# Kernel tuning notes

Measured on AMD Instinct MI355X. Metric: run time of the kernel, lower is better.

The kernel has to match this reference:

```python
import jax, jax.numpy as jnp
import numpy as np

N_HEAD, D_K, D_V, D_MODEL = 8, 64, 64, 512
LN_EPS = 1e-5

def setup_inputs() -> dict:
    key = jax.random.key(0)
    k1, k2, k3 = jax.random.split(key, 3)
    B, C, H, W = 8, D_MODEL, 32, 32
    q = jax.random.normal(k1, (B, C, H, W), dtype=jnp.float32)
    w_qkvs = jax.random.normal(k2, (N_HEAD * D_K, D_MODEL), dtype=jnp.float32) * np.sqrt(2.0 / (D_MODEL + D_K))
    fc_w = jax.random.normal(k3, (D_MODEL, N_HEAD * D_V), dtype=jnp.float32) * np.sqrt(2.0 / (N_HEAD * D_V + D_MODEL))
    fc_b = jnp.zeros((D_MODEL,), dtype=jnp.float32)
    ln_gamma = jnp.ones((D_MODEL,), dtype=jnp.float32)
    ln_beta = jnp.zeros((D_MODEL,), dtype=jnp.float32)
    return {"q": q, "w_qkvs": w_qkvs, "fc_w": fc_w, "fc_b": fc_b,
            "ln_gamma": ln_gamma, "ln_beta": ln_beta}

def reference(q, w_qkvs, fc_w, fc_b, ln_gamma, ln_beta):
    B, C, H, W = q.shape
    L = H * W
    temp = np.sqrt(D_K).astype(np.float32)
    # [B, C, H, W] -> [B, L, C] tokens
    x = q.reshape(B, C, L).transpose(0, 2, 1)
    residual = x
    # shared QKV projection -> per-head [B, h, L, d]
    qh = (x @ w_qkvs.T).reshape(B, L, N_HEAD, D_K).transpose(0, 2, 1, 3)
    # self-attention: q = k = v = qh
    scores = jnp.einsum('bhqd,bhkd->bhqk', qh, qh) / temp
    attn = jax.nn.softmax(scores, axis=-1)  # dropout is identity in eval
    out = jnp.einsum('bhqk,bhkd->bhqd', attn, qh)  # [B, h, L, d_v]
    # merge heads: [B, L, h*d_v]
    out = out.transpose(0, 2, 1, 3).reshape(B, L, N_HEAD * D_V)
    out = out @ fc_w.T + fc_b
    y = out + residual
    mu = jnp.mean(y, axis=-1, keepdims=True)
    var = jnp.mean(jnp.square(y - mu), axis=-1, keepdims=True)
    y = (y - mu) / jnp.sqrt(var + LN_EPS) * ln_gamma + ln_beta
    # raw reshape, matching torch .view(B, -1, H, W)
    return y.reshape(B, -1, H, W)
```

## Files before the change

kernel.cpp:

```cpp
#include <hip/hip_runtime.h>
#include <stdint.h>

#define BATCH 8
#define LTOK 1024
#define DMODEL 512
#define NHEAD 8
#define DHEAD 64

typedef unsigned short u16;
typedef u16 u16x4 __attribute__((ext_vector_type(4)));
typedef u16 u16x8 __attribute__((ext_vector_type(8)));
typedef short bf16x8 __attribute__((ext_vector_type(8)));
typedef float f32x4 __attribute__((ext_vector_type(4)));

#define MFMA16(a,b,c) __builtin_amdgcn_mfma_f32_16x16x32_bf16((a),(b),(c),0,0,0)

__device__ __forceinline__ float bf2f(u16 x){
  union{unsigned u; float f;} v; v.u = ((unsigned)x)<<16; return v.f;
}
__device__ __forceinline__ u16 f2bf(float f){
  union{float f; unsigned u;} v; v.f = f;
  unsigned r = v.u + 0x7fffu + ((v.u>>16)&1u);
  return (u16)(r>>16);
}

__device__ __forceinline__ void gload_lds16(const u16* g, u16* l){
  __builtin_amdgcn_global_load_lds(
      (const __attribute__((address_space(1))) void*)g,
      (__attribute__((address_space(3))) void*)l,
      16, 0, 0);
}

__global__ __launch_bounds__(256) void convert2_k(const float* __restrict__ s0,
                                                  u16* __restrict__ d0,
                                                  const float* __restrict__ s1,
                                                  u16* __restrict__ d1){
  const int blk = blockIdx.x;
  const float* src = (blk < 128) ? s0 : s1;
  u16* dst        = (blk < 128) ? d0 : d1;
  const int i = (((blk & 127)*256) + threadIdx.x)*8;
  u16x8 v;
  #pragma unroll
  for (int j=0;j<8;j++) v[j] = f2bf(src[i+j]);
  *(u16x8*)(dst + i) = v;
}

__global__ __launch_bounds__(256) void transpose_f2b(const float* __restrict__ src,
                                                     u16* __restrict__ dst,
                                                     int R, int C){
  __shared__ __align__(16) u16 t[64][72];
  const int b  = blockIdx.z;
  const int r0 = blockIdx.x*64, c0 = blockIdx.y*64;
  const float* s = src + (size_t)b*R*C;
  u16* d         = dst + (size_t)b*R*C;
  const int tid = threadIdx.x;
  const int row = tid>>3, ch = (tid&7)*8;
  #pragma unroll
  for (int rr=0; rr<64; rr+=32){
    const float* p = s + (size_t)(r0+row+rr)*C + c0 + ch;
    u16x8 v;
    #pragma unroll
    for (int j=0;j<8;j++) v[j] = f2bf(p[j]);
    *(u16x8*)&t[row+rr][ch] = v;
  }
  __syncthreads();
  #pragma unroll
  for (int rr=0; rr<64; rr+=32){
    const int dr = row+rr;
    u16x8 v;
    #pragma unroll
    for (int j=0;j<8;j++) v[j] = t[ch+j][dr];
    *(u16x8*)(d + (size_t)(c0+dr)*R + r0 + ch) = v;
  }
}

__device__ __forceinline__ void stage_gemm(const u16* __restrict__ src,
                                           int row0, int k0, u16* lds, int tid){
  #pragma unroll
  for (int s2=0; s2<2; ++s2){
    const int slot = tid + s2*256;
    const int row = slot>>3, ch8 = slot&7;
    const int k = k0 + ((ch8 ^ (row&7))<<3);
    gload_lds16(src + (size_t)(row0+row)*DMODEL + k, lds + slot*8);
  }
}

__global__ __launch_bounds__(256) void qkv_gemm(const u16* __restrict__ A,
                                                const u16* __restrict__ W,
                                                u16* __restrict__ Kf,
                                                u16* __restrict__ Vf){
  __shared__ __align__(128) u16 sA[2][4096];
  __shared__ __align__(128) u16 sB[2][4096];
  const int m0 = blockIdx.x*64, n0 = blockIdx.y*64;
  const int tid = threadIdx.x, w = tid>>6, lane = tid&63;
  const int wr = w>>1, wc = w&1;
  const int lr = lane&15, lg = lane>>4;
  f32x4 acc[2][2] = {};
  stage_gemm(A, m0, 0, sA[0], tid);
  stage_gemm(W, n0, 0, sB[0], tid);
  int buf = 0;
  for (int kt=0; kt<8; ++kt){
    __syncthreads();
    if (kt < 7){
      stage_gemm(A, m0, (kt+1)*64, sA[buf^1], tid);
      stage_gemm(W, n0, (kt+1)*64, sB[buf^1], tid);
    }
    #pragma unroll
    for (int ks=0; ks<2; ++ks){
      bf16x8 af[2], bfr[2];
      #pragma unroll
      for (int mi=0; mi<2; ++mi){
        const int r = wr*32 + mi*16 + lr;
        af[mi] = *(const bf16x8*)(&sA[buf][(r*64 + ks*32 + lg*8) ^ ((r&7)<<3)]);
      }
      #pragma unroll
      for (int nj=0; nj<2; ++nj){
        const int r = wc*32 + nj*16 + lr;
        bfr[nj] = *(const bf16x8*)(&sB[buf][(r*64 + ks*32 + lg*8) ^ ((r&7)<<3)]);
      }
      #pragma unroll
      for (int mi=0; mi<2; ++mi)
        #pragma unroll
        for (int nj=0; nj<2; ++nj)
          acc[mi][nj] = MFMA16(af[mi], bfr[nj], acc[mi][nj]);
    }
    buf ^= 1;
  }
  u16* lK = sA[0];
  u16* lV = sB[0];
  #pragma unroll
  for (int mi=0; mi<2; ++mi)
    #pragma unroll
    for (int nj=0; nj<2; ++nj){
      const int d   = wc*32 + nj*16 + lr;
      const int rr0 = wr*32 + mi*16 + lg*4;
      #pragma unroll
      for (int r=0; r<4; ++r){
        const int rr = rr0 + r;
        lK[((d>>5)*4 + (rr>>4))*512 + (((d>>3)&3)*16 + (rr&15))*8 + (d&7)]
            = f2bf(acc[mi][nj][r]);
      }
      u16x4 pv;
      #pragma unroll
      for (int r=0; r<4; ++r) pv[r] = f2bf(acc[mi][nj][r]);
      *(u16x4*)&lV[((rr0>>5)*4 + (d>>4))*512 + (((rr0>>3)&3)*16 + (d&15))*8 + (rr0&7)] = pv;
    }
  __syncthreads();
  const int bb = m0>>10, t = (m0&1023)>>6, hh = n0>>6;
  u16* Kt = Kf + (size_t)(((bb*NHEAD+hh)*16) + t)*4096;
  u16* Vt = Vf + (size_t)(((bb*NHEAD+hh)*16) + t)*4096;
  #pragma unroll
  for (int it=0; it<2; ++it){
    const int off = tid*8 + it*2048;
    *(u16x8*)(Kt + off) = *(const u16x8*)(lK + off);
    *(u16x8*)(Vt + off) = *(const u16x8*)(lV + off);
  }
}

__global__ __launch_bounds__(256,2) void attn_k(const u16* __restrict__ kf,
                                                const u16* __restrict__ vf,
                                                u16* __restrict__ ao){
  __shared__ __align__(16) u16 sPm[16640];
  const int bid = blockIdx.x;
  const int qt = bid >> 6, bh = bid & 63;
  const int b = bh >> 3, h = bh & 7;
  const u16* Kf = kf + (size_t)bh*16*4096;
  const u16* Vf = vf + (size_t)bh*16*4096;
  const int tid = threadIdx.x, w = tid>>6, lane = tid&63;
  const int lr = lane&15, lg = lane>>4;

  bf16x8 aq[4][2];
  #pragma unroll
  for (int g=0; g<4; ++g)
    #pragma unroll
    for (int ks=0; ks<2; ++ks){
      u16x8 v = *(const u16x8*)(Kf + (size_t)qt*4096 + (ks*4+g)*512 + lane*8);
      bf16x8 t;
      #pragma unroll
      for (int j=0;j<8;j++) t[j] = (short)f2bf(bf2f(v[j])*0.18033688f);
      aq[g][ks] = t;
    }

  f32x4 o[4][4] = {};
  float lsum[4][4] = {};

  for (int t=0; t<4; ++t){
    const int kt = w + t*4;
    const u16* Kt = Kf + (size_t)kt*4096;
    const u16* Vt = Vf + (size_t)kt*4096;
    bf16x8 bk[2][4];
    #pragma unroll
    for (int ks=0; ks<2; ++ks)
      #pragma unroll
      for (int nj=0; nj<4; ++nj)
        bk[ks][nj] = *(const bf16x8*)(Kt + (ks*4+nj)*512 + lane*8);
    #pragma unroll
    for (int g=0; g<4; ++g){
      f32x4 sc[4] = {};
      __builtin_amdgcn_s_setprio(1);
      #pragma unroll
      for (int ks=0; ks<2; ++ks)
        #pragma unroll
        for (int nj=0; nj<4; ++nj)
          sc[nj] = MFMA16(aq[g][ks], bk[ks][nj], sc[nj]);
      __builtin_amdgcn_s_setprio(0);
      const int wp = (w*4+g)*1024;
      #pragma unroll
      for (int nj=0; nj<4; ++nj){
        #pragma unroll
        for (int r=0; r<4; ++r){
          const float p = __builtin_amdgcn_exp2f(sc[nj][r]);
          const unsigned pu = __float_as_uint(p) & 0xFFFF0000u;
          lsum[g][r] += __uint_as_float(pu);
          const int prow = lg*4 + r;
          sPm[wp + ((prow*64 + nj*16 + lr) ^ ((prow&7)<<3))] = (u16)(pu>>16);
        }
      }
    }
    asm volatile("s_waitcnt lgkmcnt(0)" ::: "memory");
    bf16x8 bv[2][4];
    #pragma unroll
    for (int ks=0; ks<2; ++ks)
      #pragma unroll
      for (int dj=0; dj<4; ++dj)
        bv[ks][dj] = *(const bf16x8*)(Vt + (ks*4+dj)*512 + lane*8);
    __builtin_amdgcn_s_setprio(1);
    #pragma unroll
    for (int g=0; g<4; ++g){
      const int wp = (w*4+g)*1024;
      #pragma unroll
      for (int ks=0; ks<2; ++ks){
        bf16x8 pa = *(const bf16x8*)(&sPm[wp + ((lr*64 + ks*32 + lg*8) ^ ((lr&7)<<3))]);
        #pragma unroll
        for (int dj=0; dj<4; ++dj)
          o[g][dj] = MFMA16(pa, bv[ks][dj], o[g][dj]);
      }
    }
    __builtin_amdgcn_s_setprio(0);
  }

  #pragma unroll
  for (int g=0; g<4; ++g)
    #pragma unroll
    for (int r=0; r<4; ++r){
      float s = lsum[g][r];
      s += __shfl_xor(s,1); s += __shfl_xor(s,2);
      s += __shfl_xor(s,4); s += __shfl_xor(s,8);
      lsum[g][r] = s;
    }

  __syncthreads();
  float* mrg = (float*)sPm;
  if (w & 1){
    float* R = mrg + (w>>1)*4160;
    #pragma unroll
    for (int g=0; g<4; ++g){
      #pragma unroll
      for (int dj=0; dj<4; ++dj)
        *(f32x4*)&R[(g*4+dj)*256 + lane*4] = o[g][dj];
      if (lr == 0)
        #pragma unroll
        for (int r=0; r<4; ++r) R[4096 + g*16 + lg*4 + r] = lsum[g][r];
    }
  }
  __syncthreads();
  if (!(w & 1)){
    float* R = mrg + (w>>1)*4160;
    #pragma unroll
    for (int g=0; g<4; ++g){
      #pragma unroll
      for (int dj=0; dj<4; ++dj)
        o[g][dj] += *(const f32x4*)&R[(g*4+dj)*256 + lane*4];
      #pragma unroll
      for (int r=0; r<4; ++r) lsum[g][r] += R[4096 + g*16 + lg*4 + r];
    }
  }
  if (w == 2){
    float* R = mrg + 4160;
    #pragma unroll
    for (int g=0; g<4; ++g){
      #pragma unroll
      for (int dj=0; dj<4; ++dj)
        *(f32x4*)&R[(g*4+dj)*256 + lane*4] = o[g][dj];
      if (lr == 0)
        #pragma unroll
        for (int r=0; r<4; ++r) R[4096 + g*16 + lg*4 + r] = lsum[g][r];
    }
  }
  __syncthreads();
  if (w == 0){
    float* R = mrg + 4160;
    #pragma unroll
    for (int g=0; g<4; ++g){
      #pragma unroll
      for (int dj=0; dj<4; ++dj)
        o[g][dj] += *(const f32x4*)&R[(g*4+dj)*256 + lane*4];
      #pragma unroll
      for (int r=0; r<4; ++r) lsum[g][r] += R[4096 + g*16 + lg*4 + r];
    }
    #pragma unroll
    for (int g=0; g<4; ++g){
      float inv[4];
      #pragma unroll
      for (int r=0; r<4; ++r) inv[r] = __builtin_amdgcn_rcpf(lsum[g][r]);
      const int i0 = qt*64 + g*16;
      #pragma unroll
      for (int dj=0; dj<4; ++dj)
        #pragma unroll
        for (int r=0; r<4; ++r){
          const int l = i0 + lg*4 + r;
          const int d = dj*16 + lr;
          ao[((size_t)(b*LTOK + l))*DMODEL + h*DHEAD + d] = f2bf(o[g][dj][r]*inv[r]);
        }
    }
  }
}

__global__ __launch_bounds__(256) void fc_gemm(const u16* __restrict__ A,
                                               const u16* __restrict__ W,
                                               const float* __restrict__ bias,
                                               const u16* __restrict__ resid,
                                               u16* __restrict__ Y){
  __shared__ __align__(128) u16 sA[2][4096];
  __shared__ __align__(128) u16 sB[2][4096];
  const int m0 = blockIdx.x*64, n0 = blockIdx.y*64;
  const int tid = threadIdx.x, w = tid>>6, lane = tid&63;
  const int wr = w>>1, wc = w&1;
  const int lr = lane&15, lg = lane>>4;
  f32x4 acc[2][2] = {};
  stage_gemm(A, m0, 0, sA[0], tid);
  stage_gemm(W, n0, 0, sB[0], tid);
  int buf = 0;
  for (int kt=0; kt<8; ++kt){
    __syncthreads();
    if (kt < 7){
      stage_gemm(A, m0, (kt+1)*64, sA[buf^1], tid);
      stage_gemm(W, n0, (kt+1)*64, sB[buf^1], tid);
    }
    #pragma unroll
    for (int ks=0; ks<2; ++ks){
      bf16x8 af[2], bfr[2];
      #pragma unroll
      for (int mi=0; mi<2; ++mi){
        const int r = wr*32 + mi*16 + lr;
        af[mi] = *(const bf16x8*)(&sA[buf][(r*64 + ks*32 + lg*8) ^ ((r&7)<<3)]);
      }
      #pragma unroll
      for (int nj=0; nj<2; ++nj){
        const int r = wc*32 + nj*16 + lr;
        bfr[nj] = *(const bf16x8*)(&sB[buf][(r*64 + ks*32 + lg*8) ^ ((r&7)<<3)]);
      }
      #pragma unroll
      for (int mi=0; mi<2; ++mi)
        #pragma unroll
        for (int nj=0; nj<2; ++nj)
          acc[mi][nj] = MFMA16(af[mi], bfr[nj], acc[mi][nj]);
    }
    buf ^= 1;
  }
  float* lY = (float*)sA;
  #pragma unroll
  for (int mi=0; mi<2; ++mi)
    #pragma unroll
    for (int nj=0; nj<2; ++nj)
      #pragma unroll
      for (int r=0; r<4; ++r){
        const int rr = wr*32 + mi*16 + lg*4 + r;
        const int d  = wc*32 + nj*16 + lr;
        lY[(rr*64 + d) ^ ((rr&7)<<3)] = acc[mi][nj][r];
      }
  __syncthreads();
  #pragma unroll
  for (int it=0; it<2; ++it){
    const int row = (tid>>3) + it*32;
    const int ch  = (tid&7)*8;
    const int idx = (row*64 + ch) ^ ((row&7)<<3);
    f32x4 y0 = *(const f32x4*)&lY[idx];
    f32x4 y1 = *(const f32x4*)&lY[idx+4];
    u16x8 rs = *(const u16x8*)(resid + (size_t)(m0+row)*DMODEL + n0 + ch);
    u16x8 o8;
    #pragma unroll
    for (int j=0;j<4;j++) o8[j]   = f2bf(y0[j] + bias[n0+ch+j]   + bf2f(rs[j]));
    #pragma unroll
    for (int j=0;j<4;j++) o8[j+4] = f2bf(y1[j] + bias[n0+ch+4+j] + bf2f(rs[j+4]));
    *(u16x8*)(Y + (size_t)(m0+row)*DMODEL + n0 + ch) = o8;
  }
}

__global__ __launch_bounds__(256) void ln_k(const u16* __restrict__ Y,
                                            const float* __restrict__ gamma,
                                            const float* __restrict__ beta,
                                            float* __restrict__ out){
  const int row = blockIdx.x*4 + (threadIdx.x>>6);
  const int lane = threadIdx.x&63;
  const u16* yr = Y + (size_t)row*DMODEL;
  u16x8 v = *(const u16x8*)(yr + lane*8);
  float x[8]; float s=0.f, sq=0.f;
  #pragma unroll
  for (int j=0;j<8;j++){ x[j]=bf2f(v[j]); s+=x[j]; sq+=x[j]*x[j]; }
  #pragma unroll
  for (int mk=1; mk<64; mk<<=1){ s += __shfl_xor(s,mk); sq += __shfl_xor(sq,mk); }
  const float mean = s*(1.f/DMODEL);
  float var = sq*(1.f/DMODEL) - mean*mean;
  const float rstd = rsqrtf(var + 1e-5f);
  float* po = out + (size_t)row*DMODEL + lane*8;
  #pragma unroll
  for (int j=0;j<8;j++){
    const int c = lane*8+j;
    po[j] = (x[j]-mean)*rstd*gamma[c] + beta[c];
  }
}

extern "C" void kernel_launch(void* const* d_in, const int* in_sizes, int n_in,
                              void* d_out, int out_size, void* d_ws, size_t ws_size,
                              hipStream_t stream){
  (void)in_sizes; (void)n_in; (void)out_size; (void)ws_size;
  const float* q      = (const float*)d_in[0];
  const float* w_qkvs = (const float*)d_in[1];
  const float* fc_w   = (const float*)d_in[2];
  const float* fc_b   = (const float*)d_in[3];
  const float* ln_g   = (const float*)d_in[4];
  const float* ln_b   = (const float*)d_in[5];
  float* out = (float*)d_out;
  char* ws = (char*)d_ws;
  u16* x_rm  = (u16*)(ws);
  u16* kfb   = (u16*)(ws + 8388608);
  u16* vfb   = (u16*)(ws + 16777216);
  u16* ao    = (u16*)(ws + 25165824);
  u16* wqkvb = (u16*)(ws + 33554432);
  u16* wfcb  = (u16*)(ws + 34078720);
  u16* y0    = kfb;

  convert2_k<<<256,256,0,stream>>>(w_qkvs, wqkvb, fc_w, wfcb);
  transpose_f2b<<<dim3(8,16,BATCH),256,0,stream>>>(q, x_rm, DMODEL, LTOK);
  qkv_gemm<<<dim3(128,8),256,0,stream>>>(x_rm, wqkvb, kfb, vfb);
  attn_k<<<1024,256,0,stream>>>(kfb, vfb, ao);
  fc_gemm<<<dim3(128,8),256,0,stream>>>(ao, wfcb, fc_b, x_rm, y0);
  ln_k<<<2048,256,0,stream>>>(y0, ln_g, ln_b, out);
}
```

Before: 76.11 us.

## Enlarge QKV and FC GEMM block tiles from 64x64 to 128x128

Both GEMM kernels now compute 128x128 output tiles per block, with each wave holding a 64x64 sub-tile (4x4 MFMA accumulators) instead of 32x32. The goal is more operand reuse per LDS load and less global traffic per output. The epilogues are rewritten so that each wave writes its own K/V 64x64 tile and the FC output is staged with a new 128-wide swizzle. In exchange, the grid shrinks from 1024 to 256 blocks, which is about one block per CU on a 256-CU part, and register and LDS use per block rise.

Measured after the change: 74.55 us. 2.0% less time.

```diff
diff --git a/kernel.cpp b/kernel.cpp
--- a/kernel.cpp
+++ b/kernel.cpp
@@ -74,10 +74,10 @@
   }
 }
 
-__device__ __forceinline__ void stage_gemm(const u16* __restrict__ src,
-                                           int row0, int k0, u16* lds, int tid){
-  #pragma unroll
-  for (int s2=0; s2<2; ++s2){
+__device__ __forceinline__ void stage128(const u16* __restrict__ src,
+                                         int row0, int k0, u16* lds, int tid){
+  #pragma unroll
+  for (int s2=0; s2<4; ++s2){
     const int slot = tid + s2*256;
     const int row = slot>>3, ch8 = slot&7;
     const int k = k0 + ((ch8 ^ (row&7))<<3);
@@ -89,71 +89,73 @@
                                                 const u16* __restrict__ W,
                                                 u16* __restrict__ Kf,
                                                 u16* __restrict__ Vf){
-  __shared__ __align__(128) u16 sA[2][4096];
-  __shared__ __align__(128) u16 sB[2][4096];
-  const int m0 = blockIdx.x*64, n0 = blockIdx.y*64;
+  __shared__ __align__(128) u16 smem[32768];
+  const int m0 = blockIdx.x*128, n0 = blockIdx.y*128;
   const int tid = threadIdx.x, w = tid>>6, lane = tid&63;
   const int wr = w>>1, wc = w&1;
   const int lr = lane&15, lg = lane>>4;
-  f32x4 acc[2][2] = {};
-  stage_gemm(A, m0, 0, sA[0], tid);
-  stage_gemm(W, n0, 0, sB[0], tid);
+  f32x4 acc[4][4] = {};
+  stage128(A, m0, 0, smem, tid);
+  stage128(W, n0, 0, smem + 16384, tid);
   int buf = 0;
   for (int kt=0; kt<8; ++kt){
     __syncthreads();
     if (kt < 7){
-      stage_gemm(A, m0, (kt+1)*64, sA[buf^1], tid);
-      stage_gemm(W, n0, (kt+1)*64, sB[buf^1], tid);
-    }
+      stage128(A, m0, (kt+1)*64, smem + (buf^1)*8192, tid);
+      stage128(W, n0, (kt+1)*64, smem + 16384 + (buf^1)*8192, tid);
+    }
+    const u16* sa = smem + buf*8192;
+    const u16* sb = smem + 16384 + buf*8192;
     #pragma unroll
     for (int ks=0; ks<2; ++ks){
-      bf16x8 af[2], bfr[2];
-      #pragma unroll
-      for (int mi=0; mi<2; ++mi){
-        const int r = wr*32 + mi*16 + lr;
-        af[mi] = *(const bf16x8*)(&sA[buf][(r*64 + ks*32 + lg*8) ^ ((r&7)<<3)]);
-      }
-      #pragma unroll
-      for (int nj=0; nj<2; ++nj){
-        const int r = wc*32 + nj*16 + lr;
-        bfr[nj] = *(const bf16x8*)(&sB[buf][(r*64 + ks*32 + lg*8) ^ ((r&7)<<3)]);
-      }
-      #pragma unroll
-      for (int mi=0; mi<2; ++mi)
-        #pragma unroll
-        for (int nj=0; nj<2; ++nj)
+      bf16x8 af[4], bfr[4];
+      #pragma unroll
+      for (int mi=0; mi<4; ++mi){
+        const int r = wr*64 + mi*16 + lr;
+        af[mi] = *(const bf16x8*)(&sa[(r*64 + ks*32 + lg*8) ^ ((r&7)<<3)]);
+      }
+      #pragma unroll
+      for (int nj=0; nj<4; ++nj){
+        const int r = wc*64 + nj*16 + lr;
+        bfr[nj] = *(const bf16x8*)(&sb[(r*64 + ks*32 + lg*8) ^ ((r&7)<<3)]);
+      }
+      #pragma unroll
+      for (int mi=0; mi<4; ++mi)
+        #pragma unroll
+        for (int nj=0; nj<4; ++nj)
           acc[mi][nj] = MFMA16(af[mi], bfr[nj], acc[mi][nj]);
     }
     buf ^= 1;
   }
-  u16* lK = sA[0];
-  u16* lV = sB[0];
-  #pragma unroll
-  for (int mi=0; mi<2; ++mi)
-    #pragma unroll
-    for (int nj=0; nj<2; ++nj){
-      const int d   = wc*32 + nj*16 + lr;
-      const int rr0 = wr*32 + mi*16 + lg*4;
+  __syncthreads();
+  u16* Ktile = smem + w*4096;
+  u16* Vtile = smem + 16384 + w*4096;
+  #pragma unroll
+  for (int mi=0; mi<4; ++mi)
+    #pragma unroll
+    for (int nj=0; nj<4; ++nj){
+      const int rrb = mi*16 + lg*4;
+      const int d   = nj*16 + lr;
       #pragma unroll
       for (int r=0; r<4; ++r){
-        const int rr = rr0 + r;
-        lK[((d>>5)*4 + (rr>>4))*512 + (((d>>3)&3)*16 + (rr&15))*8 + (d&7)]
+        const int rr = rrb + r;
+        Ktile[((d>>5)*4 + (rr>>4))*512 + (((d>>3)&3)*16 + (rr&15))*8 + (d&7)]
             = f2bf(acc[mi][nj][r]);
       }
       u16x4 pv;
       #pragma unroll
       for (int r=0; r<4; ++r) pv[r] = f2bf(acc[mi][nj][r]);
-      *(u16x4*)&lV[((rr0>>5)*4 + (d>>4))*512 + (((rr0>>3)&3)*16 + (d&15))*8 + (rr0&7)] = pv;
-    }
-  __syncthreads();
-  const int bb = m0>>10, t = (m0&1023)>>6, hh = n0>>6;
-  u16* Kt = Kf + (size_t)(((bb*NHEAD+hh)*16) + t)*4096;
-  u16* Vt = Vf + (size_t)(((bb*NHEAD+hh)*16) + t)*4096;
-  #pragma unroll
-  for (int it=0; it<2; ++it){
-    const int off = tid*8 + it*2048;
-    *(u16x8*)(Kt + off) = *(const u16x8*)(lK + off);
-    *(u16x8*)(Vt + off) = *(const u16x8*)(lV + off);
+      *(u16x4*)&Vtile[((rrb>>5)*4 + (d>>4))*512 + (((rrb>>3)&3)*16 + (d&15))*8 + (rrb&7)] = pv;
+    }
+  __syncthreads();
+  const int bb = m0>>10, t0 = (m0&1023)>>6, hh0 = n0>>6;
+  #pragma unroll
+  for (int p=0; p<8; ++p){
+    const int gi = p*2048 + tid*8;
+    const int lt = gi>>12, off = gi&4095;
+    const size_t base = (size_t)((bb*NHEAD + hh0 + (lt&1))*16 + t0 + (lt>>1))*4096 + off;
+    *(u16x8*)(Kf + base) = *(const u16x8*)(smem + gi);
+    *(u16x8*)(Vf + base) = *(const u16x8*)(smem + 16384 + gi);
   }
 }
 
@@ -321,68 +323,71 @@
                                                const float* __restrict__ bias,
                                                const u16* __restrict__ resid,
                                                u16* __restrict__ Y){
-  __shared__ __align__(128) u16 sA[2][4096];
-  __shared__ __align__(128) u16 sB[2][4096];
-  const int m0 = blockIdx.x*64, n0 = blockIdx.y*64;
+  __shared__ __align__(128) u16 smem[32768];
+  const int m0 = blockIdx.x*128, n0 = blockIdx.y*128;
   const int tid = threadIdx.x, w = tid>>6, lane = tid&63;
   const int wr = w>>1, wc = w&1;
   const int lr = lane&15, lg = lane>>4;
-  f32x4 acc[2][2] = {};
-  stage_gemm(A, m0, 0, sA[0], tid);
-  stage_gemm(W, n0, 0, sB[0], tid);
+  f32x4 acc[4][4] = {};
+  stage128(A, m0, 0, smem, tid);
+  stage128(W, n0, 0, smem + 16384, tid);
   int buf = 0;
   for (int kt=0; kt<8; ++kt){
     __syncthreads();
     if (kt < 7){
-      stage_gemm(A, m0, (kt+1)*64, sA[buf^1], tid);
-      stage_gemm(W, n0, (kt+1)*64, sB[buf^1], tid);
-    }
+      stage128(A, m0, (kt+1)*64, smem + (buf^1)*8192, tid);
+      stage128(W, n0, (kt+1)*64, smem + 16384 + (buf^1)*8192, tid);
+    }
+    const u16* sa = smem + buf*8192;
+    const u16* sb = smem + 16384 + buf*8192;
     #pragma unroll
     for (int ks=0; ks<2; ++ks){
-      bf16x8 af[2], bfr[2];
-      #pragma unroll
-      for (int mi=0; mi<2; ++mi){
-        const int r = wr*32 + mi*16 + lr;
-        af[mi] = *(const bf16x8*)(&sA[buf][(r*64 + ks*32 + lg*8) ^ ((r&7)<<3)]);
-      }
-      #pragma unroll
-      for (int nj=0; nj<2; ++nj){
-        const int r = wc*32 + nj*16 + lr;
-        bfr[nj] = *(const bf16x8*)(&sB[buf][(r*64 + ks*32 + lg*8) ^ ((r&7)<<3)]);
-      }
-      #pragma unroll
-      for (int mi=0; mi<2; ++mi)
-        #pragma unroll
-        for (int nj=0; nj<2; ++nj)
+      bf16x8 af[4], bfr[4];
+      #pragma unroll
+      for (int mi=0; mi<4; ++mi){
+        const int r = wr*64 + mi*16 + lr;
+        af[mi] = *(const bf16x8*)(&sa[(r*64 + ks*32 + lg*8) ^ ((r&7)<<3)]);
+      }
+      #pragma unroll
+      for (int nj=0; nj<4; ++nj){
+        const int r = wc*64 + nj*16 + lr;
+        bfr[nj] = *(const bf16x8*)(&sb[(r*64 + ks*32 + lg*8) ^ ((r&7)<<3)]);
+      }
+      #pragma unroll
+      for (int mi=0; mi<4; ++mi)
+        #pragma unroll
+        for (int nj=0; nj<4; ++nj)
           acc[mi][nj] = MFMA16(af[mi], bfr[nj], acc[mi][nj]);
     }
     buf ^= 1;
   }
-  float* lY = (float*)sA;
-  #pragma unroll
-  for (int mi=0; mi<2; ++mi)
-    #pragma unroll
-    for (int nj=0; nj<2; ++nj)
+  __syncthreads();
+  float* lY = (float*)smem;
+  #pragma unroll
+  for (int mi=0; mi<4; ++mi)
+    #pragma unroll
+    for (int nj=0; nj<4; ++nj)
       #pragma unroll
       for (int r=0; r<4; ++r){
-        const int rr = wr*32 + mi*16 + lg*4 + r;
-        const int d  = wc*32 + nj*16 + lr;
-        lY[(rr*64 + d) ^ ((rr&7)<<3)] = acc[mi][nj][r];
-      }
-  __syncthreads();
-  #pragma unroll
-  for (int it=0; it<2; ++it){
-    const int row = (tid>>3) + it*32;
-    const int ch  = (tid&7)*8;
-    const int idx = (row*64 + ch) ^ ((row&7)<<3);
-    f32x4 y0 = *(const f32x4*)&lY[idx];
-    f32x4 y1 = *(const f32x4*)&lY[idx+4];
+        const int rr = wr*64 + mi*16 + lg*4 + r;
+        const int d  = wc*64 + nj*16 + lr;
+        lY[rr*128 + (d ^ ((rr&7)<<2))] = acc[mi][nj][r];
+      }
+  __syncthreads();
+  #pragma unroll
+  for (int p=0; p<8; ++p){
+    const int slot = p*256 + tid;
+    const int row = slot>>4;
+    const int ch  = (slot&15)*8;
+    const int x   = (row&7)<<2;
+    f32x4 ya = *(const f32x4*)&lY[row*128 + (ch ^ x)];
+    f32x4 yb = *(const f32x4*)&lY[row*128 + ((ch+4) ^ x)];
     u16x8 rs = *(const u16x8*)(resid + (size_t)(m0+row)*DMODEL + n0 + ch);
     u16x8 o8;
     #pragma unroll
-    for (int j=0;j<4;j++) o8[j]   = f2bf(y0[j] + bias[n0+ch+j]   + bf2f(rs[j]));
-    #pragma unroll
-    for (int j=0;j<4;j++) o8[j+4] = f2bf(y1[j] + bias[n0+ch+4+j] + bf2f(rs[j+4]));
+    for (int j=0;j<4;j++) o8[j]   = f2bf(ya[j] + bias[n0+ch+j]   + bf2f(rs[j]));
+    #pragma unroll
+    for (int j=0;j<4;j++) o8[j+4] = f2bf(yb[j] + bias[n0+ch+4+j] + bf2f(rs[j+4]));
     *(u16x8*)(Y + (size_t)(m0+row)*DMODEL + n0 + ch) = o8;
   }
 }
@@ -433,8 +438,8 @@
 
   convert2_k<<<256,256,0,stream>>>(w_qkvs, wqkvb, fc_w, wfcb);
   transpose_f2b<<<dim3(8,16,BATCH),256,0,stream>>>(q, x_rm, DMODEL, LTOK);
-  qkv_gemm<<<dim3(128,8),256,0,stream>>>(x_rm, wqkvb, kfb, vfb);
+  qkv_gemm<<<dim3(64,4),256,0,stream>>>(x_rm, wqkvb, kfb, vfb);
   attn_k<<<1024,256,0,stream>>>(kfb, vfb, ao);
-  fc_gemm<<<dim3(128,8),256,0,stream>>>(ao, wfcb, fc_b, x_rm, y0);
+  fc_gemm<<<dim3(64,4),256,0,stream>>>(ao, wfcb, fc_b, x_rm, y0);
   ln_k<<<2048,256,0,stream>>>(y0, ln_g, ln_b, out);
 }
```
